# Optimization experiments

Measured on AMD Instinct MI355X. Metric: run time of the kernel, lower is better.

The kernel has to match this reference:

```python
import jax, jax.numpy as jnp
import numpy as np

TEMPERATURE = 0.5
EPS = 1e-8  # F.cosine_similarity default eps
NEG_FILL = -1e9  # fill_diagonal_(-1000000000.0)


def setup_inputs() -> dict:
    key = jax.random.key(0)
    k1, k2 = jax.random.split(key)
    N, D = 4096, 256
    zi = jax.random.normal(k1, (N, D), dtype=jnp.float32)
    zj = jax.random.normal(k2, (N, D), dtype=jnp.float32)
    return {"zi": zi, "zj": zj}


def reference(zi, zj):
    N = zi.shape[0]
    z = jnp.concatenate([zi, zj], axis=0)  # [2N, D]
    # cosine similarity: normalize once, then a single GEMM
    norms = jnp.sqrt(jnp.sum(z * z, axis=1, keepdims=True))
    zn = z / jnp.maximum(norms, EPS)
    sim = jnp.matmul(zn, zn.T) / TEMPERATURE  # [2N, 2N]
    idx = jnp.arange(2 * N)
    sim = sim.at[idx, idx].set(NEG_FILL)  # mask self-similarity
    labels = jnp.concatenate([jnp.arange(N) + N, jnp.arange(N)])
    # CrossEntropyLoss(reduction='sum'): sum_i (logsumexp(row_i) - row_i[label_i])
    logp = jax.nn.log_softmax(sim, axis=1)
    loss = -jnp.sum(logp[idx, labels])
    return loss / (2 * N)
```

## Files before the change

kernel.cpp:

```cpp
#include <hip/hip_runtime.h>
#include <hip/hip_bf16.h>
#include <math.h>


using short8  = __attribute__((ext_vector_type(8))) short;
using floatx4 = __attribute__((ext_vector_type(4))) float;

constexpr int TWO_N = 8192;
constexpr int DIM   = 256;
constexpr int NB    = 64;
constexpr int NTRI  = NB * (NB + 1) / 2;
constexpr float INV2N = 1.0f / 8192.0f;

__device__ static inline unsigned short f2bf(float f) {
  unsigned u = __float_as_uint(f);
  return (unsigned short)((u + 0x7fffu + ((u >> 16) & 1u)) >> 16);
}

__device__ static inline void async_copy16(const __hip_bfloat16* g, __hip_bfloat16* l) {
  __builtin_amdgcn_global_load_lds(
      (const __attribute__((address_space(1))) void*)(const void*)g,
      (__attribute__((address_space(3))) void*)(void*)l, 16, 0, 0);
}

__global__ __launch_bounds__(256) void k_normalize(
    const float* __restrict__ zi, const float* __restrict__ zj,
    __hip_bfloat16* __restrict__ zn, float* __restrict__ rowtotal,
    float* __restrict__ out)
{
  if (blockIdx.x == 0 && threadIdx.x == 0) out[0] = 0.0f;
  if (blockIdx.x < 32) rowtotal[blockIdx.x * 256 + threadIdx.x] = 0.0f;

  const int lane = threadIdx.x & 63;
  const int wave = threadIdx.x >> 6;
  const int row  = blockIdx.x * 4 + wave;
  const float* src = (row < 4096) ? (zi + (size_t)row * DIM)
                                  : (zj + (size_t)(row - 4096) * DIM);
  float4 v = reinterpret_cast<const float4*>(src)[lane];
  float ss = v.x * v.x + v.y * v.y + v.z * v.z + v.w * v.w;
#pragma unroll
  for (int m = 32; m >= 1; m >>= 1) ss += __shfl_xor(ss, m, 64);
  float inv = 1.0f / fmaxf(sqrtf(ss), 1e-8f);
  ushort4 o;
  o.x = f2bf(v.x * inv); o.y = f2bf(v.y * inv);
  o.z = f2bf(v.z * inv); o.w = f2bf(v.w * inv);
  reinterpret_cast<ushort4*>(zn + (size_t)row * DIM)[lane] = o;
}

__global__ __launch_bounds__(256) void k_simexp(
    const __hip_bfloat16* __restrict__ Z, float* __restrict__ rowtotal,
    float* __restrict__ out)
{
  __shared__ __align__(16) __hip_bfloat16 As[128 * 64];
  __shared__ __align__(16) __hip_bfloat16 Bs[128 * 64];
  __shared__ float rowsum[128];
  __shared__ float colsum[128];

  const int tid  = threadIdx.x;
  const int lane = tid & 63;
  const int wave = tid >> 6;
  const int wm   = wave >> 1;
  const int wn   = wave & 1;

  const int u = blockIdx.x;
  int jb = (int)((sqrtf(8.0f * (float)u + 1.0f) - 1.0f) * 0.5f);
  while ((jb + 1) * (jb + 2) / 2 <= u) ++jb;
  while (jb * (jb + 1) / 2 > u) --jb;
  const int ib = u - jb * (jb + 1) / 2;

  const bool diagblk = (ib == jb);
  const bool pairblk = (jb == ib + 32);
  const int i0 = ib * 128;
  const int j0 = jb * 128;

  if (tid < 128) { rowsum[tid] = 0.0f; colsum[tid] = 0.0f; }

  floatx4 acc[4][4] = {};

  const int lane7 = lane & 7;
  const int sub   = lane >> 3;
  const int gkoff = ((lane7 ^ sub) << 3);
  const int q     = lane >> 4;
  const int c16   = lane & 15;

  const __hip_bfloat16* gbase =
      Z + (size_t)((wave < 2 ? i0 : j0) + (wave & 1) * 64) * DIM;
  __hip_bfloat16* lbase = ((wave < 2) ? As : Bs) + (wave & 1) * 64 * 64;

  for (int kk = 0; kk < 4; ++kk) {
    const int k0 = kk * 64;
#pragma unroll
    for (int c = 0; c < 8; ++c) {
      const __hip_bfloat16* gp = gbase + (size_t)(c * 8 + sub) * DIM + k0 + gkoff;
      async_copy16(gp, lbase + c * 512);
    }
    __syncthreads();

#pragma unroll
    for (int ks = 0; ks < 2; ++ks) {
      const int phys = (ks * 4 + q) ^ lane7;
      short8 a[4], b[4];
#pragma unroll
      for (int mt = 0; mt < 4; ++mt)
        a[mt] = *reinterpret_cast<const short8*>(
            As + (wm * 64 + mt * 16 + c16) * 64 + phys * 8);
#pragma unroll
      for (int nt = 0; nt < 4; ++nt)
        b[nt] = *reinterpret_cast<const short8*>(
            Bs + (wn * 64 + nt * 16 + c16) * 64 + phys * 8);
#pragma unroll
      for (int mt = 0; mt < 4; ++mt)
#pragma unroll
        for (int nt = 0; nt < 4; ++nt)
          acc[mt][nt] = __builtin_amdgcn_mfma_f32_16x16x32_bf16(
              a[mt], b[nt], acc[mt][nt], 0, 0, 0);
    }
    __syncthreads();
  }

  float colacc[4] = {0.f, 0.f, 0.f, 0.f};
  float pc = 0.f;
  const bool diagwave = (wm == wn);

#pragma unroll
  for (int mt = 0; mt < 4; ++mt) {
#pragma unroll
    for (int reg = 0; reg < 4; ++reg) {
      const bool onquad = (c16 == q * 4 + reg);
      float s = 0.0f;
#pragma unroll
      for (int nt = 0; nt < 4; ++nt) {
        float e = __expf(2.0f * acc[mt][nt][reg] - 2.0f);
        bool skip = diagblk && diagwave && (nt == mt) && onquad;
        s += skip ? 0.0f : e;
        colacc[nt] += e;
      }
      if (pairblk && diagwave && onquad) pc += acc[mt][mt][reg];
      s += __shfl_xor(s, 1, 64);
      s += __shfl_xor(s, 2, 64);
      s += __shfl_xor(s, 4, 64);
      s += __shfl_xor(s, 8, 64);
      if (c16 == 0)
        atomicAdd(&rowsum[wm * 64 + mt * 16 + q * 4 + reg], s);
    }
  }

  if (!diagblk) {
#pragma unroll
    for (int nt = 0; nt < 4; ++nt) {
      float cs = colacc[nt];
      cs += __shfl_xor(cs, 16, 64);
      cs += __shfl_xor(cs, 32, 64);
      if (lane < 16) atomicAdd(&colsum[wn * 64 + nt * 16 + lane], cs);
    }
  }

  if (pairblk && diagwave) {
#pragma unroll
    for (int m = 32; m >= 1; m >>= 1) pc += __shfl_xor(pc, m, 64);
    if (lane == 0) atomicAdd(out, -4.0f * pc * INV2N);
  }

  __syncthreads();
  if (tid < 128) {
    atomicAdd(&rowtotal[i0 + tid], rowsum[tid]);
    if (!diagblk) atomicAdd(&rowtotal[j0 + tid], colsum[tid]);
  }
}

__global__ __launch_bounds__(256) void k_finalize(
    const float* __restrict__ rowtotal, float* __restrict__ out)
{
  __shared__ float wsum[4];
  const int lane = threadIdx.x & 63;
  const int wave = threadIdx.x >> 6;
  const int row  = blockIdx.x * 256 + threadIdx.x;
  float v = 2.0f + __logf(rowtotal[row]);
#pragma unroll
  for (int m = 32; m >= 1; m >>= 1) v += __shfl_xor(v, m, 64);
  if (lane == 0) wsum[wave] = v;
  __syncthreads();
  if (threadIdx.x == 0)
    atomicAdd(out, (wsum[0] + wsum[1] + wsum[2] + wsum[3]) * INV2N);
}

extern "C" void kernel_launch(void* const* d_in, const int* in_sizes, int n_in,
                              void* d_out, int out_size, void* d_ws, size_t ws_size,
                              hipStream_t stream) {
  const float* zi = (const float*)d_in[0];
  const float* zj = (const float*)d_in[1];
  float* out = (float*)d_out;

  __hip_bfloat16* zn = (__hip_bfloat16*)d_ws;
  float* rowtotal = (float*)((char*)d_ws + (size_t)TWO_N * DIM * 2);

  k_normalize<<<dim3(TWO_N / 4), dim3(256), 0, stream>>>(zi, zj, zn, rowtotal, out);
  k_simexp<<<dim3(NTRI), dim3(256), 0, stream>>>(zn, rowtotal, out);
  k_finalize<<<dim3(TWO_N / 256), dim3(256), 0, stream>>>(rowtotal, out);
}
```

Baseline: 103.8 us.

## Double-buffer K tiles in sim GEMM and replace global atomics with partial-sum matrix

The GEMM main loop now uses two LDS buffers of 32-wide K slices, so the async load of the next slice is issued while the current one is consumed, with one barrier per step instead of two. Per-row exp sums are no longer accumulated with global atomicAdd into a row-total array. Each tile writes its partial into a [2N x 64] matrix indexed by block column, and the finalize kernel reduces each row with a wave-wide shuffle before the log. This removes atomic contention and the zeroing step, at the cost of extra workspace and a heavier finalize pass.

```diff
diff --git a/kernel.cpp b/kernel.cpp
--- a/kernel.cpp
+++ b/kernel.cpp
@@ -25,12 +25,9 @@
 
 __global__ __launch_bounds__(256) void k_normalize(
     const float* __restrict__ zi, const float* __restrict__ zj,
-    __hip_bfloat16* __restrict__ zn, float* __restrict__ rowtotal,
-    float* __restrict__ out)
+    __hip_bfloat16* __restrict__ zn, float* __restrict__ out)
 {
   if (blockIdx.x == 0 && threadIdx.x == 0) out[0] = 0.0f;
-  if (blockIdx.x < 32) rowtotal[blockIdx.x * 256 + threadIdx.x] = 0.0f;
-
   const int lane = threadIdx.x & 63;
   const int wave = threadIdx.x >> 6;
   const int row  = blockIdx.x * 4 + wave;
@@ -48,11 +45,11 @@
 }
 
 __global__ __launch_bounds__(256) void k_simexp(
-    const __hip_bfloat16* __restrict__ Z, float* __restrict__ rowtotal,
+    const __hip_bfloat16* __restrict__ Z, float* __restrict__ P,
     float* __restrict__ out)
 {
-  __shared__ __align__(16) __hip_bfloat16 As[128 * 64];
-  __shared__ __align__(16) __hip_bfloat16 Bs[128 * 64];
+  __shared__ __align__(16) __hip_bfloat16 Ab[2][128 * 32];
+  __shared__ __align__(16) __hip_bfloat16 Bb[2][128 * 32];
   __shared__ float rowsum[128];
   __shared__ float colsum[128];
 
@@ -61,6 +58,8 @@
   const int wave = tid >> 6;
   const int wm   = wave >> 1;
   const int wn   = wave & 1;
+  const int c16  = lane & 15;
+  const int q    = lane >> 4;
 
   const int u = blockIdx.x;
   int jb = (int)((sqrtf(8.0f * (float)u + 1.0f) - 1.0f) * 0.5f);
@@ -77,46 +76,45 @@
 
   floatx4 acc[4][4] = {};
 
-  const int lane7 = lane & 7;
-  const int sub   = lane >> 3;
-  const int gkoff = ((lane7 ^ sub) << 3);
-  const int q     = lane >> 4;
-  const int c16   = lane & 15;
-
+  const int rloc  = lane >> 2;
+  const int koff  = ((lane & 3) ^ (rloc & 3)) << 3;
   const __hip_bfloat16* gbase =
       Z + (size_t)((wave < 2 ? i0 : j0) + (wave & 1) * 64) * DIM;
-  __hip_bfloat16* lbase = ((wave < 2) ? As : Bs) + (wave & 1) * 64 * 64;
-
-  for (int kk = 0; kk < 4; ++kk) {
-    const int k0 = kk * 64;
-#pragma unroll
-    for (int c = 0; c < 8; ++c) {
-      const __hip_bfloat16* gp = gbase + (size_t)(c * 8 + sub) * DIM + k0 + gkoff;
-      async_copy16(gp, lbase + c * 512);
-    }
+  const int lhalf = (wave & 1) * 64 * 32;
+
+#define STAGE(buf_, k0_)                                                      \
+  do {                                                                        \
+    __hip_bfloat16* lb = ((wave < 2) ? Ab[buf_] : Bb[buf_]) + lhalf;          \
+    _Pragma("unroll") for (int c = 0; c < 4; ++c)                             \
+        async_copy16(gbase + (size_t)(c * 16 + rloc) * DIM + (k0_) + koff,    \
+                     lb + c * 512);                                           \
+  } while (0)
+
+  STAGE(0, 0);
+#pragma unroll
+  for (int kk = 0; kk < 8; ++kk) {
+    const int cur = kk & 1;
     __syncthreads();
-
-#pragma unroll
-    for (int ks = 0; ks < 2; ++ks) {
-      const int phys = (ks * 4 + q) ^ lane7;
-      short8 a[4], b[4];
-#pragma unroll
-      for (int mt = 0; mt < 4; ++mt)
-        a[mt] = *reinterpret_cast<const short8*>(
-            As + (wm * 64 + mt * 16 + c16) * 64 + phys * 8);
+    if (kk < 7) STAGE(cur ^ 1, (kk + 1) * 32);
+
+    const int phys = q ^ (c16 & 3);
+    short8 a[4], b[4];
+#pragma unroll
+    for (int mt = 0; mt < 4; ++mt)
+      a[mt] = *reinterpret_cast<const short8*>(
+          Ab[cur] + (wm * 64 + mt * 16 + c16) * 32 + phys * 8);
+#pragma unroll
+    for (int nt = 0; nt < 4; ++nt)
+      b[nt] = *reinterpret_cast<const short8*>(
+          Bb[cur] + (wn * 64 + nt * 16 + c16) * 32 + phys * 8);
+#pragma unroll
+    for (int mt = 0; mt < 4; ++mt)
 #pragma unroll
       for (int nt = 0; nt < 4; ++nt)
-        b[nt] = *reinterpret_cast<const short8*>(
-            Bs + (wn * 64 + nt * 16 + c16) * 64 + phys * 8);
-#pragma unroll
-      for (int mt = 0; mt < 4; ++mt)
-#pragma unroll
-        for (int nt = 0; nt < 4; ++nt)
-          acc[mt][nt] = __builtin_amdgcn_mfma_f32_16x16x32_bf16(
-              a[mt], b[nt], acc[mt][nt], 0, 0, 0);
-    }
-    __syncthreads();
-  }
+        acc[mt][nt] = __builtin_amdgcn_mfma_f32_16x16x32_bf16(
+            a[mt], b[nt], acc[mt][nt], 0, 0, 0);
+  }
+#undef STAGE
 
   float colacc[4] = {0.f, 0.f, 0.f, 0.f};
   float pc = 0.f;
@@ -163,22 +161,27 @@
 
   __syncthreads();
   if (tid < 128) {
-    atomicAdd(&rowtotal[i0 + tid], rowsum[tid]);
-    if (!diagblk) atomicAdd(&rowtotal[j0 + tid], colsum[tid]);
+    P[(size_t)(i0 + tid) * 64 + jb] = rowsum[tid];
+    if (!diagblk) P[(size_t)(j0 + tid) * 64 + ib] = colsum[tid];
   }
 }
 
 __global__ __launch_bounds__(256) void k_finalize(
-    const float* __restrict__ rowtotal, float* __restrict__ out)
+    const float* __restrict__ P, float* __restrict__ out)
 {
   __shared__ float wsum[4];
   const int lane = threadIdx.x & 63;
   const int wave = threadIdx.x >> 6;
-  const int row  = blockIdx.x * 256 + threadIdx.x;
-  float v = 2.0f + __logf(rowtotal[row]);
-#pragma unroll
-  for (int m = 32; m >= 1; m >>= 1) v += __shfl_xor(v, m, 64);
-  if (lane == 0) wsum[wave] = v;
+  float acc = 0.0f;
+#pragma unroll
+  for (int it = 0; it < 16; ++it) {
+    const int r = blockIdx.x * 64 + it * 4 + wave;
+    float s = P[(size_t)r * 64 + lane];
+#pragma unroll
+    for (int m = 32; m >= 1; m >>= 1) s += __shfl_xor(s, m, 64);
+    if (lane == 0) acc += 2.0f + __logf(s);
+  }
+  if (lane == 0) wsum[wave] = acc;
   __syncthreads();
   if (threadIdx.x == 0)
     atomicAdd(out, (wsum[0] + wsum[1] + wsum[2] + wsum[3]) * INV2N);
@@ -192,9 +195,9 @@
   float* out = (float*)d_out;
 
   __hip_bfloat16* zn = (__hip_bfloat16*)d_ws;
-  float* rowtotal = (float*)((char*)d_ws + (size_t)TWO_N * DIM * 2);
-
-  k_normalize<<<dim3(TWO_N / 4), dim3(256), 0, stream>>>(zi, zj, zn, rowtotal, out);
-  k_simexp<<<dim3(NTRI), dim3(256), 0, stream>>>(zn, rowtotal, out);
-  k_finalize<<<dim3(TWO_N / 256), dim3(256), 0, stream>>>(rowtotal, out);
-}
+  float* P = (float*)((char*)d_ws + (size_t)TWO_N * DIM * 2);
+
+  k_normalize<<<dim3(TWO_N / 4), dim3(256), 0, stream>>>(zi, zj, zn, out);
+  k_simexp<<<dim3(NTRI), dim3(256), 0, stream>>>(zn, P, out);
+  k_finalize<<<dim3(TWO_N / 64), dim3(256), 0, stream>>>(P, out);
+}
```

Result: slower. 109.9 us (+5.9%).
